# Kernel tuning notes

Hardware: AMD Instinct MI355X
Metric: run time of the kernel (lower is better)

The kernel has to match this reference:

```python
import jax, jax.numpy as jnp
import numpy as np

S, B, C, H, W = 16, 64, 128, 11, 11
P = H * W
N_ITER = 3
EPS = 1e-5


def setup_inputs() -> dict:
    key = jax.random.key(0)
    ks = jax.random.split(key, 12)
    w = lambda k, shape: jax.random.normal(k, shape, jnp.float32) * 0.02
    return {
        "x": jax.random.normal(ks[0], (S, B, C, H, W), jnp.float32),
        # intra-attention 1x1 convs (stored as [out,in] matrices)
        "wq": w(ks[1], (C, C)), "bq": jnp.zeros((C,), jnp.float32),
        "wk": w(ks[2], (C, C)), "bk": jnp.zeros((C,), jnp.float32),
        "wv": w(ks[3], (C, C)), "bv": jnp.zeros((C,), jnp.float32),
        "intra_alpha": jnp.float32(1.0),
        # inter-message path
        "w_msg": w(ks[4], (C, C + 1)), "b_msg": jnp.zeros((C,), jnp.float32),
        "w_lin": w(ks[5], (C, C)),
        "weight": jnp.float32(0.5),
        "w_gate": w(ks[6], (C, C)), "b_gate": jnp.zeros((C,), jnp.float32),
        # ConvGRU 3x3 convs
        "w_zr": w(ks[7], (2 * C, 2 * C, 3, 3)), "b_zr": jnp.zeros((2 * C,), jnp.float32),
        "w_h": w(ks[8], (C, 2 * C, 3, 3)), "b_h": jnp.zeros((C,), jnp.float32),
        # LayerNorm over [C,11,11]
        "ln_gamma": jnp.ones((C, H, W), jnp.float32),
        "ln_beta": jnp.zeros((C, H, W), jnp.float32),
    }


def reference(x, wq, bq, wk, bk, wv, bv, intra_alpha, w_msg, b_msg, w_lin,
              weight, w_gate, b_gate, w_zr, b_zr, w_h, b_h, ln_gamma, ln_beta):
    scale = C ** -0.5

    def c1(t, wgt, bias):  # 1x1 conv on [S,B,Cin,H,W] -> [S,B,Cout,H,W]
        return jnp.einsum('sbchw,oc->sbohw', t, wgt) + bias[:, None, None]

    def conv3(t, wgt, bias):  # 3x3 'SAME' conv on [N,Cin,H,W]
        y = jax.lax.conv_general_dilated(
            t, wgt, (1, 1), 'SAME', dimension_numbers=('NCHW', 'OIHW', 'NCHW'))
        return y + bias[None, :, None, None]

    # chain-graph neighbor validity masks (|i-j| == 1)
    mask_l = (jnp.arange(S) >= 1).astype(x.dtype)[:, None, None, None, None]
    mask_r = (jnp.arange(S) <= S - 2).astype(x.dtype)[:, None, None, None, None]

    h = x
    for _ in range(N_ITER):
        # ---- intra spatial self-attention (per node, over P=H*W tokens) ----
        q = c1(h, wq, bq).reshape(S, B, C, P)
        k = c1(h, wk, bk).reshape(S, B, C, P)
        v = c1(h, wv, bv).reshape(S, B, C, P)
        att = jax.nn.softmax(jnp.einsum('sbcp,sbcq->sbpq', q, k) * scale, axis=-1)
        intra = jnp.einsum('sbpq,sbcq->sbcp', att, v).reshape(S, B, C, H, W)
        intra = intra_alpha * intra + h

        # ---- inter gated message attention from chain neighbors ----
        xf = h.reshape(S, B, C, P)

        def gated_msg(y, edge_val):
            ef = jnp.full((S, B, 1, H, W), edge_val, h.dtype)  # edge feature i-j
            yy = c1(jnp.concatenate([y, ef], axis=2), w_msg, b_msg).reshape(S, B, C, P)
            yy = jnp.einsum('sbcp,dc->sbdp', yy, w_lin)  # Linear (no bias)
            a = jax.nn.softmax(jnp.einsum('sbcp,sbcq->sbpq', xf, yy), axis=-1)
            m = jnp.einsum('sbpq,sbcq->sbcp', a, yy).reshape(S, B, C, H, W)
            g = jax.nn.sigmoid(c1(m, w_gate, b_gate).mean(axis=(-2, -1), keepdims=True))
            return m * g

        y_left = jnp.concatenate([jnp.zeros_like(h[:1]), h[:-1]], axis=0)   # h[i-1], edge +1
        y_right = jnp.concatenate([h[1:], jnp.zeros_like(h[:1])], axis=0)   # h[i+1], edge -1
        inter = gated_msg(y_left, 1.0) * mask_l + gated_msg(y_right, -1.0) * mask_r

        comb = weight * intra + (1.0 - weight) * inter

        # ---- ConvGRU update (fold S into batch) ----
        xg = comb.reshape(S * B, C, H, W)
        hg = h.reshape(S * B, C, H, W)
        zr = jax.nn.sigmoid(conv3(jnp.concatenate([xg, hg], axis=1), w_zr, b_zr))
        z, r = zr[:, :C], zr[:, C:]
        h_hat = jnp.tanh(conv3(jnp.concatenate([xg, r * hg], axis=1), w_h, b_h))
        h_new = ((1 - z) * hg + z * h_hat).reshape(S, B, C, H, W)

        # ---- residual + LayerNorm over [C,H,W] ----
        nh = h_new + h
        mu = nh.mean(axis=(-3, -2, -1), keepdims=True)
        var = nh.var(axis=(-3, -2, -1), keepdims=True)
        h = (nh - mu) * jax.lax.rsqrt(var + EPS) * ln_gamma + ln_beta
    return h
```

## Files before the change

### kernel.cpp

```cpp
#include <hip/hip_runtime.h>
#include <hip/hip_bf16.h>

#define S_   16
#define B_   64
#define SBn  1024
#define C_   128
#define P_   121
#define CP_  15488
#define LTS  17408
static const long NEl = 15859712L;

typedef __hip_bfloat16 bf16t;
typedef __attribute__((ext_vector_type(8))) short bf16x8;
typedef __attribute__((ext_vector_type(4))) float f32x4;
typedef __attribute__((ext_vector_type(4))) unsigned short us4;

__device__ __forceinline__ float ldb(const bf16t* p){ return __bfloat162float(*p); }
__device__ __forceinline__ float b2f(unsigned short u){ unsigned x=((unsigned)u)<<16; float f; __builtin_memcpy(&f,&x,4); return f; }
__device__ __forceinline__ unsigned short f2bu(float v){ __hip_bfloat16 b=__float2bfloat16(v); unsigned short u; __builtin_memcpy(&u,&b,2); return u; }
__device__ __forceinline__ float ldin(const void* s, long i, int f){
    return f ? ((const float*)s)[i] : b2f(((const unsigned short*)s)[i]);
}

__global__ void detect_kernel(const unsigned short* __restrict__ x, int* __restrict__ flag){
// ... 264 lines not shown
    #pragma unroll
    for(int io=0;io<2;io++){
        f32x4 acc[4][2];
        gemm24r(acc,WqT,hreg[io],ocr,l15,kg);
        #pragma unroll
        for(int mt=0;mt<4;mt++){
            int oc0=ocr*64+mt*16+kg*4;
            #pragma unroll
            for(int nt=0;nt<2;nt++){
                int p=pcr*32+nt*16+l15;
                us4 pk;
                #pragma unroll
                for(int r=0;r<4;r++) pk[r]=f2bu(acc[mt][nt][r]+bq[oc0+r]);
                *(us4*)(LA[io]+p*136+oc0)=pk;
            }
        }
        gemm24r(acc,WkT,hreg[io],ocr,l15,kg);
        #pragma unroll
        for(int mt=0;mt<4;mt++){
            int oc0=ocr*64+mt*16+kg*4;
            #pragma unroll
            for(int nt=0;nt<2;nt++){
                int p=pcr*32+nt*16+l15;
                us4 pk;
                #pragma unroll
                for(int r=0;r<4;r++) pk[r]=f2bu(acc[mt][nt][r]+bk[oc0+r]);
                *(us4*)(LB[io]+p*136+oc0)=pk;
            }
        }
    }
    __syncthreads();
    const float scale=0.08838834764831845f;
    f32x4 s[2][8];
    #pragma unroll
    for(int io=0;io<2;io++){
        #pragma unroll
        for(int nt=0;nt<8;nt++) s[io][nt]=(f32x4){0.f,0.f,0.f,0.f};
        #pragma unroll
        for(int kc=0;kc<4;kc++){
            bf16x8 a=*(const bf16x8*)(LA[io]+(size_t)(m0+l15)*136+kc*32+kg*8);
            #pragma unroll
            for(int nt=0;nt<8;nt++){
                bf16x8 b=*(const bf16x8*)(LB[io]+(size_t)(nt*16+l15)*136+kc*32+kg*8);
                s[io][nt]=__builtin_amdgcn_mfma_f32_16x16x32_bf16(a,b,s[io][nt],0,0,0);
            }
        }
        #pragma unroll
        for(int nt=0;nt<8;nt++){
            #pragma unroll
            for(int r=0;r<4;r++) s[io][nt][r]*=scale;
        }
        if(l15>=9){
            #pragma unroll
            for(int r=0;r<4;r++) s[io][7][r]=-3.0e38f;
        }
        #pragma unroll
        for(int r=0;r<4;r++){
            float mx=s[io][0][r];
            #pragma unroll
            for(int nt=1;nt<8;nt++) mx=fmaxf(mx,s[io][nt][r]);
            #pragma unroll
            for(int o=1;o<16;o<<=1) mx=fmaxf(mx,__shfl_xor(mx,o));
            float sm=0.f;
            #pragma unroll
            for(int nt=0;nt<8;nt++){ float e=__expf(s[io][nt][r]-mx); s[io][nt][r]=e; sm+=e; }
            #pragma unroll
            for(int o=1;o<16;o<<=1) sm+=__shfl_xor(sm,o);
            float rs=1.f/sm;
            #pragma unroll
            for(int nt=0;nt<8;nt++) s[io][nt][r]*=rs;
        }
    }
    __syncthreads();
    #pragma unroll
    for(int io=0;io<2;io++){
        f32x4 acc[4][2];
        gemm24r(acc,WvT,hreg[io],ocr,l15,kg);
        #pragma unroll
        for(int mt=0;mt<4;mt++){
            int oc0=ocr*64+mt*16+kg*4;
            #pragma unroll
            for(int nt=0;nt<2;nt++){
                int p=pcr*32+nt*16+l15;
                #pragma unroll
                for(int r=0;r<4;r++)
                    LA[io][(oc0+r)*136+p]=__float2bfloat16(p<P_? acc[mt][nt][r]+bv[oc0+r] : 0.f);
            }
        }
        #pragma unroll
        for(int r=0;r<4;r++){
            int pr=m0+kg*4+r;
            #pragma unroll
            for(int nt=0;nt<8;nt++) LB[io][pr*136+nt*16+l15]=__float2bfloat16(s[io][nt][r]);
        }
    }
    __syncthreads();
    float al=*alphap, wv=*wp, w1m=1.f-wv;
    int c0=m0+kg*4;
    f32x4 res[2][8];
    #pragma unroll
    for(int io=0;io<2;io++){
        #pragma unroll
        for(int nt=0;nt<8;nt++) res[io][nt]=(f32x4){0.f,0.f,0.f,0.f};
        #pragma unroll
        for(int jc=0;jc<4;jc++){
            bf16x8 a=*(const bf16x8*)(LA[io]+(size_t)(m0+l15)*136+jc*32+kg*8);
            #pragma unroll
            for(int nt=0;nt<8;nt++){
                bf16x8 b=*(const bf16x8*)(LB[io]+(size_t)(nt*16+l15)*136+jc*32+kg*8);
                res[io][nt]=__builtin_amdgcn_mfma_f32_16x16x32_bf16(a,b,res[io][nt],0,0,0);
            }
        }
        const bf16t* hp=(io==0)?hp0:hp1;
        #pragma unroll
        for(int nt=0;nt<8;nt++){
            int p=nt*16+l15;
            int pc=(p<P_)?p:(P_-1);
            us4 hv=*(const us4*)(hp+(size_t)pc*C_+c0);
            #pragma unroll
            for(int r=0;r<4;r++) res[io][nt][r]=wv*(al*res[io][nt][r]+b2f(hv[r]));
        }
    }
    if(sb0>=B_)
        msg_phase2(res,hT,sb0,-B_,W2T,b2l,wgT,bgf,w1m,areg,LA,LB,fl,t,w,l15,kg,ocr,pcr);
    if(sb0<SBn-B_)
        msg_phase2(res,hT,sb0, B_,W2T,b2r,wgT,bgf,w1m,areg,LA,LB,fl,t,w,l15,kg,ocr,pcr);
    __syncthreads();
    #pragma unroll
    for(int io=0;io<2;io++){
        unsigned short* tl=(unsigned short*)LA[io];
        #pragma unroll
        for(int nt=0;nt<8;nt++){
            int p=nt*16+l15;
            if(p>=P_) continue;
            us4 pk;
            #pragma unroll
            for(int r=0;r<4;r++) pk[r]=f2bu(res[io][nt][r]);
            *(us4*)(tl+p*C_+c0)=pk;
        }
    }
    __syncthreads();
    {
        bf16t* ob0=comb+(size_t)sb0*CP_;
        const unsigned short* t0=(const unsigned short*)LA[0];
        for(int j=t;j<1936;j+=512)
            *(bf16x8*)(ob0+j*8)=*(const bf16x8*)(t0+j*8);
        bf16t* ob1=comb+(size_t)(sb0+1)*CP_;
        const unsigned short* t1=(const unsigned short*)LA[1];
        for(int j=t;j<1936;j+=512)
            *(bf16x8*)(ob1+j*8)=*(const bf16x8*)(t1+j*8);
    }
}

#define LOADA2(bidx, widx) { \
    _Pragma("unroll") \
    for(int mt=0;mt<2;mt++) abuf[bidx][mt]=*(const bf16x8*)(Wt+(size_t)(widx)*(OC*32)+mt*512+base_lane); }
#define STEP2(lbase, bidx, doff) { \
    bf16x8 bb[4]; \
    _Pragma("unroll") \
    for(int nt=0;nt<4;nt++) bb[nt]=*(const bf16x8*)((lbase)+boff[nt]+(doff)); \
    __builtin_amdgcn_s_setprio(1); \
    _Pragma("unroll") \
    for(int mt=0;mt<2;mt++){ \
        _Pragma("unroll") \
        for(int nt=0;nt<4;nt++) \
            acc[mt][nt]=__builtin_amdgcn_mfma_f32_16x16x32_bf16(abuf[bidx][mt],bb[nt],acc[mt][nt],0,0,0); } \
    __builtin_amdgcn_s_setprio(0); }

#define SLOADZ2(stg) { \
    const bf16t* s0=(((stg)<2)? in0T:in1T)+(size_t)sb0*CP_+((stg)&1)*64; \
    const bf16t* s1=s0+CP_; \
    sreg[0]=*(const bf16x8*)(s0+(size_t)spA*C_+(t&7)*8); \
    if(sv1) sreg[1]=*(const bf16x8*)(s0+(size_t)spB*C_+(t&7)*8); \
    sreg[2]=*(const bf16x8*)(s1+(size_t)spA*C_+(t&7)*8); \
    if(sv1) sreg[3]=*(const bf16x8*)(s1+(size_t)spB*C_+(t&7)*8); }
#define SWRITEZ2(lbase) { \
    *(bf16x8*)((lbase)+spixA*72+(t&7)*8)=sreg[0]; \
    if(sv1) *(bf16x8*)((lbase)+spixB*72+(t&7)*8)=sreg[1]; \
    *(bf16x8*)((lbase)+12176+spixA*72+(t&7)*8)=sreg[2]; \
    if(sv1) *(bf16x8*)((lbase)+12176+spixB*72+(t&7)*8)=sreg[3]; }
#define STEPZ2(lbase, bidx, doff) { \
    bf16x8 bb0[4], bb1[4]; \
    _Pragma("unroll") \
    for(int nt=0;nt<4;nt++){ \
        bb0[nt]=*(const bf16x8*)((lbase)+boff[nt]+(doff)); \
        bb1[nt]=*(const bf16x8*)((lbase)+12176+boff[nt]+(doff)); } \
    __builtin_amdgcn_s_setprio(1); \
    _Pragma("unroll") \
    for(int mt=0;mt<2;mt++){ \
        _Pragma("unroll") \
        for(int nt=0;nt<4;nt++){ \
            accA[mt][nt]=__builtin_amdgcn_mfma_f32_16x16x32_bf16(abuf[bidx][mt],bb0[nt],accA[mt][nt],0,0,0); \
            accB[mt][nt]=__builtin_amdgcn_mfma_f32_16x16x32_bf16(abuf[bidx][mt],bb1[nt],accB[mt][nt],0,0,0); } } \
    __builtin_amdgcn_s_setprio(0); }

__global__ __launch_bounds__(512) void conv3_zr2(
    bf16t* __restrict__ o0, bf16t* __restrict__ o1,
    const bf16t* __restrict__ in0T, const bf16t* __restrict__ in1T,
    const bf16t* __restrict__ Wt, const float* __restrict__ bias,
    const bf16t* __restrict__ hTb)
{
    constexpr int OC=256;
    __shared__ bf16t lin[4*12176];
    int sb0=(int)blockIdx.x*2, ocb=(int)blockIdx.y*128;
    int t=threadIdx.x, lane=t&63, w=t>>6;
    int ocr=w>>1, pcr=w&1, l15=lane&15, kg=lane>>4;
    int boff[4]; bool pv_[4];
    #pragma unroll
    for(int nt=0;nt<4;nt++){
        int p=pcr*64+nt*16+l15;
        pv_[nt]=(p<P_); int pc=pv_[nt]?p:(P_-1);
        boff[nt]=((pc/11)*13+(pc%11))*72+kg*8;
    }
    f32x4 accA[2][4], accB[2][4];
    #pragma unroll
    for(int i=0;i<2;i++){
        #pragma unroll
        for(int j=0;j<4;j++){ accA[i][j]=(f32x4){0.f,0.f,0.f,0.f}; accB[i][j]=(f32x4){0.f,0.f,0.f,0.f}; }
    }
    int base_lane=(ocb+ocr*32+l15)*32+kg*8;
    bf16x8 abuf[4][2];
    bf16x8 sreg[4];
    bool sv1=((t+512)<968);
    int spA=t>>3, spB=(t+512)>>3;
    if(spB>120) spB=120;
    int spixA=(spA/11+1)*13+(spA%11)+1;
    int spixB=(spB/11+1)*13+(spB%11)+1;
    LOADA2(0,0); LOADA2(1,1); LOADA2(2,8); LOADA2(3,9);
    SLOADZ2(0);
    {
        bf16x8 z;
        #pragma unroll
        for(int e=0;e<8;e++) z[e]=0;
        for(int i=t;i<1536;i+=512){
            int tile=i/384; int i2=i-tile*384;
            int bi=i2>>3, cc=(i2&7)*8;
            int pix;
            if(bi<13) pix=bi;
            else if(bi<26) pix=156+(bi-13);
            else { int j2=bi-26; pix=(1+(j2>>1))*13+((j2&1)?12:0); }
            *(bf16x8*)(lin+tile*12176+pix*72+cc)=z;
        }
    }
    SWRITEZ2(lin);
    __syncthreads();
    #pragma unroll
    for(int st=0; st<4; ++st){
        if(st<3) SLOADZ2(st+1);
        bf16t* lbase=lin+(st&1)*24352;
        #pragma unroll
        for(int k=0;k<18;k++){
            int s=st*18+k;
            int tap=k>>1, l=k&1;
            int doff=((tap/3)*13+(tap%3))*72+l*32;
            STEPZ2(lbase, s&3, doff);
            if(s<68){
                int s4=s+4, st4=s4/18, k4=s4-st4*18, tap4=k4>>1, l4=k4&1;
                LOADA2(s&3, tap4*8+st4*2+l4);
            }
        }
        if(st<3){ SWRITEZ2(lin+((st+1)&1)*24352); }
        __syncthreads();
    }
    unsigned short* tl=(unsigned short*)lin;
    bf16t* obase=(ocb==0? o0 : o1);
    const float* bs=bias+(ocb==0?0:128);
    #pragma unroll
    for(int mt=0;mt<2;mt++){
        int ocl=ocr*32+mt*16+kg*4;
        #pragma unroll
        for(int nt=0;nt<4;nt++){
            if(!pv_[nt]) continue;
            int p=pcr*64+nt*16+l15;
            us4 pk;
            if(ocb==0){
                #pragma unroll
                for(int r=0;r<4;r++){ float a=accA[mt][nt][r]+bs[ocl+r]; pk[r]=f2bu(1.f/(1.f+__expf(-a))); }
            }else{
                size_t tb=(size_t)sb0*CP_+(size_t)p*C_+ocl;
                us4 hv=*(const us4*)(hTb+tb);
                #pragma unroll
                for(int r=0;r<4;r++){ float a=accA[mt][nt][r]+bs[ocl+r]; float sg=1.f/(1.f+__expf(-a)); pk[r]=f2bu(sg*b2f(hv[r])); }
            }
            *(us4*)(tl+p*C_+ocl)=pk;
        }
    }
    __syncthreads();
    {
        bf16t* ob=obase+(size_t)sb0*CP_;
        for(int j=t;j<1936;j+=512)
            *(bf16x8*)(ob+j*8)=*(const bf16x8*)(tl+j*8);
    }
    __syncthreads();
    #pragma unroll
    for(int mt=0;mt<2;mt++){
        int ocl=ocr*32+mt*16+kg*4;
        #pragma unroll
        for(int nt=0;nt<4;nt++){
            if(!pv_[nt]) continue;
            int p=pcr*64+nt*16+l15;
            us4 pk;
            if(ocb==0){
                #pragma unroll
                for(int r=0;r<4;r++){ float a=accB[mt][nt][r]+bs[ocl+r]; pk[r]=f2bu(1.f/(1.f+__expf(-a))); }
            }else{
                size_t tb=(size_t)(sb0+1)*CP_+(size_t)p*C_+ocl;
                us4 hv=*(const us4*)(hTb+tb);
                #pragma unroll
                for(int r=0;r<4;r++){ float a=accB[mt][nt][r]+bs[ocl+r]; float sg=1.f/(1.f+__expf(-a)); pk[r]=f2bu(sg*b2f(hv[r])); }
            }
            *(us4*)(tl+p*C_+ocl)=pk;
        }
    }
    __syncthreads();
    {
        bf16t* ob=obase+(size_t)(sb0+1)*CP_;
        for(int j=t;j<1936;j+=512)
            *(bf16x8*)(ob+j*8)=*(const bf16x8*)(tl+j*8);
    }
}

#define SLOADH(stg) { \
    const bf16t* ssrc=(((stg)<2)? in0T:in1T)+(size_t)sb*CP_+((stg)&1)*64; \
    sreg[0]=*(const bf16x8*)(ssrc+(size_t)(t>>3)*C_+(t&7)*8); \
    if(sv1) sreg[1]=*(const bf16x8*)(ssrc+(size_t)sp1*C_+(t&7)*8); }
#define SWRITEH(lbase) { \
    *(bf16x8*)((lbase)+spix0*72+(t&7)*8)=sreg[0]; \
    if(sv1) *(bf16x8*)((lbase)+spix1*72+(t&7)*8)=sreg[1]; }

__global__ __launch_bounds__(512,4) void conv3_hh(
    bf16t* __restrict__ o0,
    const bf16t* __restrict__ in0T, const bf16t* __restrict__ in1T,
    const bf16t* __restrict__ Wt, const float* __restrict__ bias,
    const bf16t* __restrict__ zT, const bf16t* __restrict__ hTb,
    const float* __restrict__ gamT, const float* __restrict__ betT)
{
    constexpr int OC=128;
    __shared__ bf16t lin[2*12176];
    __shared__ float red[16];
    int sb=blockIdx.x;
    int t=threadIdx.x, lane=t&63, w=t>>6;
    int ocr=w>>1, pcr=w&1, l15=lane&15, kg=lane>>4;
    int boff[4]; bool pv_[4];
    #pragma unroll
    for(int nt=0;nt<4;nt++){
        int p=pcr*64+nt*16+l15;
        pv_[nt]=(p<P_); int pc=pv_[nt]?p:(P_-1);
        boff[nt]=((pc/11)*13+(pc%11))*72+kg*8;
    }
    f32x4 acc[2][4];
    #pragma unroll
    for(int i=0;i<2;i++){
        #pragma unroll
        for(int j=0;j<4;j++) acc[i][j]=(f32x4){0.f,0.f,0.f,0.f};
    }
    int base_lane=(ocr*32+l15)*32+kg*8;
    bf16x8 abuf[4][2];
    bf16x8 sreg[2];
    bool sv1=((t+512)<968);
    int sp0=t>>3, sp1=(t+512)>>3;
    if(sp1>120) sp1=120;
    int spix0=(sp0/11+1)*13+(sp0%11)+1;
    int spix1=(sp1/11+1)*13+(sp1%11)+1;
    LOADA2(0,0); LOADA2(1,1); LOADA2(2,8); LOADA2(3,9);
    SLOADH(0);
    {
        bf16x8 z;
        #pragma unroll
        for(int e=0;e<8;e++) z[e]=0;
        for(int i=t;i<768;i+=512){
            int half=i>=384; int i2=i-half*384;
            int bi=i2>>3, cc=(i2&7)*8;
            int pix;
            if(bi<13) pix=bi;
            else if(bi<26) pix=156+(bi-13);
            else { int j2=bi-26; pix=(1+(j2>>1))*13+((j2&1)?12:0); }
            *(bf16x8*)(lin+half*12176+pix*72+cc)=z;
        }
    }
    SWRITEH(lin);
    __syncthreads();
    #pragma unroll
    for(int st=0; st<4; ++st){
        if(st<3) SLOADH(st+1);
        bf16t* lbase=lin+(st&1)*12176;
        #pragma unroll
        for(int k=0;k<18;k++){
            int s=st*18+k;
            int tap=k>>1, l=k&1;
            int doff=((tap/3)*13+(tap%3))*72+l*32;
            STEP2(lbase, s&3, doff);
            if(s<68){
                int s4=s+4, st4=s4/18, k4=s4-st4*18, tap4=k4>>1, l4=k4&1;
                LOADA2(s&3, tap4*8+st4*2+l4);
            }
        }
        if(st<3){ SWRITEH(lin+((st+1)&1)*12176); }
        __syncthreads();
    }
    float ls=0.f, ls2=0.f;
    #pragma unroll
    for(int mt=0;mt<2;mt++){
        int ocl=ocr*32+mt*16+kg*4;
        #pragma unroll
        for(int nt=0;nt<4;nt++){
            if(!pv_[nt]) continue;
            int p=pcr*64+nt*16+l15;
            size_t tb=(size_t)sb*CP_+(size_t)p*C_+ocl;
            us4 hv=*(const us4*)(hTb+tb);
            us4 zv=*(const us4*)(zT+tb);
            us4 pk;
            #pragma unroll
            for(int r=0;r<4;r++){
                float a=acc[mt][nt][r]+bias[ocl+r];
                float ht=tanhf(a);
                float z=b2f(zv[r]), h=b2f(hv[r]);
                unsigned short u=f2bu((1.f-z)*h+z*ht+h);
                pk[r]=u;
                float nr=b2f(u); ls+=nr; ls2+=nr*nr;
            }
            *(us4*)((unsigned short*)lin + p*C_+ocl)=pk;
        }
    }
    #pragma unroll
    for(int o=32;o;o>>=1){ ls+=__shfl_xor(ls,o); ls2+=__shfl_xor(ls2,o); }
    if(lane==0){ red[w]=ls; red[8+w]=ls2; }
    __syncthreads();
    float Sx=0.f,Sx2=0.f;
    #pragma unroll
    for(int i=0;i<8;i++){ Sx+=red[i]; Sx2+=red[8+i]; }
    float mu=Sx*(1.f/(float)CP_);
    float var=Sx2*(1.f/(float)CP_)-mu*mu;
    float rstd=rsqrtf(var+1e-5f);
    bf16t* ho=o0+(size_t)sb*CP_;
    const unsigned short* tl=(const unsigned short*)lin;
    for(int j=t;j<1936;j+=512){
        int base=j*8;
        bf16x8 ovec;
        #pragma unroll
        for(int e=0;e<8;e++){
            float v=(b2f(tl[base+e])-mu)*rstd*gamT[base+e]+betT[base+e];
            ovec[e]=(short)f2bu(v);
        }
        *(bf16x8*)(ho+base)=ovec;
    }
}

__global__ __launch_bounds__(256) void finalT_kernel(void* __restrict__ fout, const bf16t* __restrict__ hT, const int* __restrict__ flag){
    __shared__ bf16t tl[CP_];
    int sb=blockIdx.x, t=threadIdx.x, f=*flag;
    for(int i=t;i<CP_;i+=256) tl[i]=hT[(size_t)sb*CP_+i];
    __syncthreads();
    for(int i=t;i<CP_;i+=256){
        int c=i/P_, p=i-c*P_;
        float v=ldb(tl+p*C_+c);
        size_t oi=(size_t)sb*CP_+i;
        if(f) ((float*)fout)[oi]=v;
        else  ((bf16t*)fout)[oi]=__float2bfloat16(v);
    }
}

extern "C" void kernel_launch(void* const* d_in, const int* in_sizes, int n_in,
                              void* d_out, int out_size, void* d_ws, size_t ws_size,
                              hipStream_t stream) {
    (void)in_sizes; (void)n_in; (void)out_size;
    char* base=(char*)d_ws;
    size_t off=0;
    auto alloc=[&](size_t bytes){ void* p=base+off; off+=(bytes+255)&~(size_t)255; return p; };
    bf16t* b1=(bf16t*)alloc((size_t)NEl*2+8192);
    bf16t* b2=(bf16t*)alloc((size_t)NEl*2+8192);
    bf16t* b3=(bf16t*)alloc((size_t)NEl*2+8192);
    bf16t* b4=(bf16t*)d_out;
    bf16t* wqT=(bf16t*)alloc(16384*2);
    bf16t* wkT=(bf16t*)alloc(16384*2);
    bf16t* wvT=(bf16t*)alloc(16384*2);
    bf16t* w2T=(bf16t*)alloc(16384*2);
    bf16t* wzrT=(bf16t*)alloc((size_t)589824*2);
    bf16t* whT =(bf16t*)alloc((size_t)294912*2);
    float* W2f=(float*)alloc(16384*4);
    float* b2l=(float*)alloc(128*4); float* b2r=(float*)alloc(128*4);
    float* bqf=(float*)alloc(128*4); float* bkf=(float*)alloc(128*4); float* bvf=(float*)alloc(128*4);
    float* bzrf=(float*)alloc(256*4); float* bhf=(float*)alloc(128*4);
    float* gamT=(float*)alloc(15488*4); float* betT=(float*)alloc(15488*4);
    float* wgTf=(float*)alloc(16384*4); float* bgf2=(float*)alloc(128*4);
    float* alphaf=(float*)alloc(4); float* weightf=(float*)alloc(4);
    int* flag=(int*)alloc(4);
    if(ws_size<off) return;

    detect_kernel<<<1,64,0,stream>>>((const unsigned short*)d_in[0],flag);
    cvtT_kernel<<<SBn,256,0,stream>>>(b1,d_in[0],flag);
    prep_w1t<1><<<64,256,0,stream>>>(wqT,d_in[1],flag);
    cvt_kernel<<<1,128,0,stream>>>(bqf,d_in[2],128,flag);
    prep_w1t<1><<<64,256,0,stream>>>(wkT,d_in[3],flag);
    cvt_kernel<<<1,128,0,stream>>>(bkf,d_in[4],128,flag);
    prep_w1t<1><<<64,256,0,stream>>>(wvT,d_in[5],flag);
    cvt_kernel<<<1,128,0,stream>>>(bvf,d_in[6],128,flag);
    cvt_kernel<<<1,64,0,stream>>>(alphaf,d_in[7],1,flag);
    prep_msg_kernel<<<C_,C_,0,stream>>>(W2f,b2l,b2r,d_in[10],d_in[8],d_in[9],flag);
    prep_w1t<0><<<64,256,0,stream>>>(w2T,W2f,flag);
    cvt_kernel<<<1,64,0,stream>>>(weightf,d_in[11],1,flag);
    prep_wgt<<<64,256,0,stream>>>(wgTf,bgf2,d_in[12],d_in[13],flag);
    prep_w3t<<<(256*2304+255)/256,256,0,stream>>>(wzrT,d_in[14],flag,256);
    cvt_kernel<<<1,256,0,stream>>>(bzrf,d_in[15],256,flag);
    prep_w3t<<<(128*2304+255)/256,256,0,stream>>>(whT,d_in[16],flag,128);
    cvt_kernel<<<1,128,0,stream>>>(bhf,d_in[17],128,flag);
    prep_gbt<<<(CP_+255)/256,256,0,stream>>>(gamT,betT,d_in[18],d_in[19],flag);

    for(int it=0; it<3; ++it){
        attn2<<<SBn/2,512,0,stream>>>(b2,b1,wqT,wkT,wvT,bqf,bkf,bvf,
                                      w2T,b2l,b2r,wgTf,bgf2,alphaf,weightf);
        conv3_zr2<<<dim3(SBn/2,2),512,0,stream>>>(b4,b3,b2,b1,wzrT,bzrf,b1);
        conv3_hh<<<SBn,512,0,stream>>>(b1,b2,b3,whT,bhf,b4,b1,gamT,betT);
    }
    finalT_kernel<<<SBn,256,0,stream>>>(d_out,b1,flag);
}
```

Baseline: 1.300 ms.

## Process two nodes per block in the h-hat conv to reuse weight fragments

After: 1.286 ms. About the same (-1.0%).

```diff
diff --git a/kernel.cpp b/kernel.cpp
--- a/kernel.cpp
+++ b/kernel.cpp
@@ -443,18 +443,6 @@
 #define LOADA2(bidx, widx) { \
     _Pragma("unroll") \
     for(int mt=0;mt<2;mt++) abuf[bidx][mt]=*(const bf16x8*)(Wt+(size_t)(widx)*(OC*32)+mt*512+base_lane); }
-#define STEP2(lbase, bidx, doff) { \
-    bf16x8 bb[4]; \
-    _Pragma("unroll") \
-    for(int nt=0;nt<4;nt++) bb[nt]=*(const bf16x8*)((lbase)+boff[nt]+(doff)); \
-    __builtin_amdgcn_s_setprio(1); \
-    _Pragma("unroll") \
-    for(int mt=0;mt<2;mt++){ \
-        _Pragma("unroll") \
-        for(int nt=0;nt<4;nt++) \
-            acc[mt][nt]=__builtin_amdgcn_mfma_f32_16x16x32_bf16(abuf[bidx][mt],bb[nt],acc[mt][nt],0,0,0); } \
-    __builtin_amdgcn_s_setprio(0); }
-
 #define SLOADZ2(stg) { \
     const bf16t* s0=(((stg)<2)? in0T:in1T)+(size_t)sb0*CP_+((stg)&1)*64; \
     const bf16t* s1=s0+CP_; \
@@ -608,15 +596,7 @@
     }
 }
 
-#define SLOADH(stg) { \
-    const bf16t* ssrc=(((stg)<2)? in0T:in1T)+(size_t)sb*CP_+((stg)&1)*64; \
-    sreg[0]=*(const bf16x8*)(ssrc+(size_t)(t>>3)*C_+(t&7)*8); \
-    if(sv1) sreg[1]=*(const bf16x8*)(ssrc+(size_t)sp1*C_+(t&7)*8); }
-#define SWRITEH(lbase) { \
-    *(bf16x8*)((lbase)+spix0*72+(t&7)*8)=sreg[0]; \
-    if(sv1) *(bf16x8*)((lbase)+spix1*72+(t&7)*8)=sreg[1]; }
-
-__global__ __launch_bounds__(512,4) void conv3_hh(
+__global__ __launch_bounds__(512) void conv3_hh2(
     bf16t* __restrict__ o0,
     const bf16t* __restrict__ in0T, const bf16t* __restrict__ in1T,
     const bf16t* __restrict__ Wt, const float* __restrict__ bias,
@@ -624,9 +604,9 @@
     const float* __restrict__ gamT, const float* __restrict__ betT)
 {
     constexpr int OC=128;
-    __shared__ bf16t lin[2*12176];
+    __shared__ bf16t lin[4*12176];
     __shared__ float red[16];
-    int sb=blockIdx.x;
+    int sb0=(int)blockIdx.x*2;
     int t=threadIdx.x, lane=t&63, w=t>>6;
     int ocr=w>>1, pcr=w&1, l15=lane&15, kg=lane>>4;
     int boff[4]; bool pv_[4];
@@ -636,101 +616,151 @@
         pv_[nt]=(p<P_); int pc=pv_[nt]?p:(P_-1);
         boff[nt]=((pc/11)*13+(pc%11))*72+kg*8;
     }
-    f32x4 acc[2][4];
+    f32x4 accA[2][4], accB[2][4];
     #pragma unroll
     for(int i=0;i<2;i++){
         #pragma unroll
-        for(int j=0;j<4;j++) acc[i][j]=(f32x4){0.f,0.f,0.f,0.f};
+        for(int j=0;j<4;j++){ accA[i][j]=(f32x4){0.f,0.f,0.f,0.f}; accB[i][j]=(f32x4){0.f,0.f,0.f,0.f}; }
     }
     int base_lane=(ocr*32+l15)*32+kg*8;
     bf16x8 abuf[4][2];
-    bf16x8 sreg[2];
+    bf16x8 sreg[4];
     bool sv1=((t+512)<968);
-    int sp0=t>>3, sp1=(t+512)>>3;
-    if(sp1>120) sp1=120;
-    int spix0=(sp0/11+1)*13+(sp0%11)+1;
-    int spix1=(sp1/11+1)*13+(sp1%11)+1;
+    int spA=t>>3, spB=(t+512)>>3;
+    if(spB>120) spB=120;
+    int spixA=(spA/11+1)*13+(spA%11)+1;
+    int spixB=(spB/11+1)*13+(spB%11)+1;
     LOADA2(0,0); LOADA2(1,1); LOADA2(2,8); LOADA2(3,9);
-    SLOADH(0);
+    SLOADZ2(0);
     {
         bf16x8 z;
         #pragma unroll
         for(int e=0;e<8;e++) z[e]=0;
-        for(int i=t;i<768;i+=512){
-            int half=i>=384; int i2=i-half*384;
+        for(int i=t;i<1536;i+=512){
+            int tile=i/384; int i2=i-tile*384;
             int bi=i2>>3, cc=(i2&7)*8;
             int pix;
             if(bi<13) pix=bi;
             else if(bi<26) pix=156+(bi-13);
             else { int j2=bi-26; pix=(1+(j2>>1))*13+((j2&1)?12:0); }
-            *(bf16x8*)(lin+half*12176+pix*72+cc)=z;
-        }
-    }
-    SWRITEH(lin);
+            *(bf16x8*)(lin+tile*12176+pix*72+cc)=z;
+        }
+    }
+    SWRITEZ2(lin);
     __syncthreads();
     #pragma unroll
     for(int st=0; st<4; ++st){
-        if(st<3) SLOADH(st+1);
-        bf16t* lbase=lin+(st&1)*12176;
+        if(st<3) SLOADZ2(st+1);
+        bf16t* lbase=lin+(st&1)*24352;
         #pragma unroll
         for(int k=0;k<18;k++){
             int s=st*18+k;
             int tap=k>>1, l=k&1;
             int doff=((tap/3)*13+(tap%3))*72+l*32;
-            STEP2(lbase, s&3, doff);
+            STEPZ2(lbase, s&3, doff);
             if(s<68){
                 int s4=s+4, st4=s4/18, k4=s4-st4*18, tap4=k4>>1, l4=k4&1;
                 LOADA2(s&3, tap4*8+st4*2+l4);
             }
         }
-        if(st<3){ SWRITEH(lin+((st+1)&1)*12176); }
+        if(st<3){ SWRITEZ2(lin+((st+1)&1)*24352); }
         __syncthreads();
     }
-    float ls=0.f, ls2=0.f;
-    #pragma unroll
-    for(int mt=0;mt<2;mt++){
-        int ocl=ocr*32+mt*16+kg*4;
-        #pragma unroll
-        for(int nt=0;nt<4;nt++){
-            if(!pv_[nt]) continue;
-            int p=pcr*64+nt*16+l15;
-            size_t tb=(size_t)sb*CP_+(size_t)p*C_+ocl;
-            us4 hv=*(const us4*)(hTb+tb);
-            us4 zv=*(const us4*)(zT+tb);
-            us4 pk;
-            #pragma unroll
-            for(int r=0;r<4;r++){
-                float a=acc[mt][nt][r]+bias[ocl+r];
-                float ht=tanhf(a);
-                float z=b2f(zv[r]), h=b2f(hv[r]);
-                unsigned short u=f2bu((1.f-z)*h+z*ht+h);
-                pk[r]=u;
-                float nr=b2f(u); ls+=nr; ls2+=nr*nr;
-            }
-            *(us4*)((unsigned short*)lin + p*C_+ocl)=pk;
-        }
-    }
-    #pragma unroll
-    for(int o=32;o;o>>=1){ ls+=__shfl_xor(ls,o); ls2+=__shfl_xor(ls2,o); }
-    if(lane==0){ red[w]=ls; red[8+w]=ls2; }
-    __syncthreads();
-    float Sx=0.f,Sx2=0.f;
-    #pragma unroll
-    for(int i=0;i<8;i++){ Sx+=red[i]; Sx2+=red[8+i]; }
-    float mu=Sx*(1.f/(float)CP_);
-    float var=Sx2*(1.f/(float)CP_)-mu*mu;
-    float rstd=rsqrtf(var+1e-5f);
-    bf16t* ho=o0+(size_t)sb*CP_;
-    const unsigned short* tl=(const unsigned short*)lin;
-    for(int j=t;j<1936;j+=512){
-        int base=j*8;
-        bf16x8 ovec;
-        #pragma unroll
-        for(int e=0;e<8;e++){
-            float v=(b2f(tl[base+e])-mu)*rstd*gamT[base+e]+betT[base+e];
-            ovec[e]=(short)f2bu(v);
-        }
-        *(bf16x8*)(ho+base)=ovec;
+    unsigned short* tl=(unsigned short*)lin;
+    {
+        float ls=0.f, ls2=0.f;
+        #pragma unroll
+        for(int mt=0;mt<2;mt++){
+            int ocl=ocr*32+mt*16+kg*4;
+            #pragma unroll
+            for(int nt=0;nt<4;nt++){
+                if(!pv_[nt]) continue;
+                int p=pcr*64+nt*16+l15;
+                size_t tb=(size_t)sb0*CP_+(size_t)p*C_+ocl;
+                us4 hv=*(const us4*)(hTb+tb);
+                us4 zv=*(const us4*)(zT+tb);
+                us4 pk;
+                #pragma unroll
+                for(int r=0;r<4;r++){
+                    float a=accA[mt][nt][r]+bias[ocl+r];
+                    float ht=tanhf(a);
+                    float z=b2f(zv[r]), h=b2f(hv[r]);
+                    unsigned short u=f2bu((1.f-z)*h+z*ht+h);
+                    pk[r]=u;
+                    float nr=b2f(u); ls+=nr; ls2+=nr*nr;
+                }
+                *(us4*)(tl+p*C_+ocl)=pk;
+            }
+        }
+        #pragma unroll
+        for(int o=32;o;o>>=1){ ls+=__shfl_xor(ls,o); ls2+=__shfl_xor(ls2,o); }
+        if(lane==0){ red[w]=ls; red[8+w]=ls2; }
+        __syncthreads();
+        float Sx=0.f,Sx2=0.f;
+        #pragma unroll
+        for(int i=0;i<8;i++){ Sx+=red[i]; Sx2+=red[8+i]; }
+        float mu=Sx*(1.f/(float)CP_);
+        float var=Sx2*(1.f/(float)CP_)-mu*mu;
+        float rstd=rsqrtf(var+1e-5f);
+        bf16t* ho=o0+(size_t)sb0*CP_;
+        for(int j=t;j<1936;j+=512){
+            int base=j*8;
+            bf16x8 ovec;
+            #pragma unroll
+            for(int e=0;e<8;e++){
+                float v=(b2f(tl[base+e])-mu)*rstd*gamT[base+e]+betT[base+e];
+                ovec[e]=(short)f2bu(v);
+            }
+            *(bf16x8*)(ho+base)=ovec;
+        }
+    }
+    __syncthreads();
+    {
+        float ls=0.f, ls2=0.f;
+        #pragma unroll
+        for(int mt=0;mt<2;mt++){
+            int ocl=ocr*32+mt*16+kg*4;
+            #pragma unroll
+            for(int nt=0;nt<4;nt++){
+                if(!pv_[nt]) continue;
+                int p=pcr*64+nt*16+l15;
+                size_t tb=(size_t)(sb0+1)*CP_+(size_t)p*C_+ocl;
+                us4 hv=*(const us4*)(hTb+tb);
+                us4 zv=*(const us4*)(zT+tb);
+                us4 pk;
+                #pragma unroll
+                for(int r=0;r<4;r++){
+                    float a=accB[mt][nt][r]+bias[ocl+r];
+                    float ht=tanhf(a);
+                    float z=b2f(zv[r]), h=b2f(hv[r]);
+                    unsigned short u=f2bu((1.f-z)*h+z*ht+h);
+                    pk[r]=u;
+                    float nr=b2f(u); ls+=nr; ls2+=nr*nr;
+                }
+                *(us4*)(tl+p*C_+ocl)=pk;
+            }
+        }
+        #pragma unroll
+        for(int o=32;o;o>>=1){ ls+=__shfl_xor(ls,o); ls2+=__shfl_xor(ls2,o); }
+        if(lane==0){ red[w]=ls; red[8+w]=ls2; }
+        __syncthreads();
+        float Sx=0.f,Sx2=0.f;
+        #pragma unroll
+        for(int i=0;i<8;i++){ Sx+=red[i]; Sx2+=red[8+i]; }
+        float mu=Sx*(1.f/(float)CP_);
+        float var=Sx2*(1.f/(float)CP_)-mu*mu;
+        float rstd=rsqrtf(var+1e-5f);
+        bf16t* ho=o0+(size_t)(sb0+1)*CP_;
+        for(int j=t;j<1936;j+=512){
+            int base=j*8;
+            bf16x8 ovec;
+            #pragma unroll
+            for(int e=0;e<8;e++){
+                float v=(b2f(tl[base+e])-mu)*rstd*gamT[base+e]+betT[base+e];
+                ovec[e]=(short)f2bu(v);
+            }
+            *(bf16x8*)(ho+base)=ovec;
+        }
     }
 }
 
@@ -798,7 +828,7 @@
         attn2<<<SBn/2,512,0,stream>>>(b2,b1,wqT,wkT,wvT,bqf,bkf,bvf,
                                       w2T,b2l,b2r,wgTf,bgf2,alphaf,weightf);
         conv3_zr2<<<dim3(SBn/2,2),512,0,stream>>>(b4,b3,b2,b1,wzrT,bzrf,b1);
-        conv3_hh<<<SBn,512,0,stream>>>(b1,b2,b3,whT,bhf,b4,b1,gamT,betT);
+        conv3_hh2<<<SBn/2,512,0,stream>>>(b1,b2,b3,whT,bhf,b4,b1,gamT,betT);
     }
     finalT_kernel<<<SBn,256,0,stream>>>(d_out,b1,flag);
 }
```

## Fuse ConvGRU gate and candidate convolutions into one kernel via LDS

Applied to the files above, without the earlier changes.

New measurement: 1.253 ms. -3.6%, faster.

```diff
diff --git a/kernel.cpp b/kernel.cpp
--- a/kernel.cpp
+++ b/kernel.cpp
@@ -440,82 +440,81 @@
     }
 }
 
-#define LOADA2(bidx, widx) { \
+#define GSB0 0
+#define GSB1 12176
+#define GSP0 24352
+#define GSP1 36528
+#define GSZ  48704
+#define SZSTR 132
+
+#define LOADAZ(bidx, widx) { \
     _Pragma("unroll") \
-    for(int mt=0;mt<2;mt++) abuf[bidx][mt]=*(const bf16x8*)(Wt+(size_t)(widx)*(OC*32)+mt*512+base_lane); }
-#define STEP2(lbase, bidx, doff) { \
+    for(int mt=0;mt<2;mt++) abuf[bidx][mt]=*(const bf16x8*)(Wzr+(size_t)(widx)*(256*32)+mt*512+base_laneZ); }
+#define LOADAH(bidx, widx) { \
+    _Pragma("unroll") \
+    for(int mt=0;mt<2;mt++) abuf[bidx][mt]=*(const bf16x8*)(Wh+(size_t)(widx)*(128*32)+mt*512+base_laneH); }
+#define STEPZ8(lbase, bidx, doff) { \
+    bf16x8 bb[8]; \
+    _Pragma("unroll") \
+    for(int nt=0;nt<8;nt++) bb[nt]=*(const bf16x8*)(lin+(lbase)+boffZ[nt]+(doff)); \
+    __builtin_amdgcn_s_setprio(1); \
+    _Pragma("unroll") \
+    for(int mt=0;mt<2;mt++){ \
+        _Pragma("unroll") \
+        for(int nt=0;nt<8;nt++) \
+            accZ[mt][nt]=__builtin_amdgcn_mfma_f32_16x16x32_bf16(abuf[bidx][mt],bb[nt],accZ[mt][nt],0,0,0); } \
+    __builtin_amdgcn_s_setprio(0); }
+#define STEPH4(lbase, bidx, doff) { \
     bf16x8 bb[4]; \
     _Pragma("unroll") \
-    for(int nt=0;nt<4;nt++) bb[nt]=*(const bf16x8*)((lbase)+boff[nt]+(doff)); \
+    for(int nt=0;nt<4;nt++) bb[nt]=*(const bf16x8*)(lin+(lbase)+boffH[nt]+(doff)); \
     __builtin_amdgcn_s_setprio(1); \
     _Pragma("unroll") \
     for(int mt=0;mt<2;mt++){ \
         _Pragma("unroll") \
         for(int nt=0;nt<4;nt++) \
-            acc[mt][nt]=__builtin_amdgcn_mfma_f32_16x16x32_bf16(abuf[bidx][mt],bb[nt],acc[mt][nt],0,0,0); } \
+            accH[mt][nt]=__builtin_amdgcn_mfma_f32_16x16x32_bf16(abuf[bidx][mt],bb[nt],accH[mt][nt],0,0,0); } \
     __builtin_amdgcn_s_setprio(0); }
-
-#define SLOADZ2(stg) { \
-    const bf16t* s0=(((stg)<2)? in0T:in1T)+(size_t)sb0*CP_+((stg)&1)*64; \
-    const bf16t* s1=s0+CP_; \
-    sreg[0]=*(const bf16x8*)(s0+(size_t)spA*C_+(t&7)*8); \
-    if(sv1) sreg[1]=*(const bf16x8*)(s0+(size_t)spB*C_+(t&7)*8); \
-    sreg[2]=*(const bf16x8*)(s1+(size_t)spA*C_+(t&7)*8); \
-    if(sv1) sreg[3]=*(const bf16x8*)(s1+(size_t)spB*C_+(t&7)*8); }
-#define SWRITEZ2(lbase) { \
-    *(bf16x8*)((lbase)+spixA*72+(t&7)*8)=sreg[0]; \
-    if(sv1) *(bf16x8*)((lbase)+spixB*72+(t&7)*8)=sreg[1]; \
-    *(bf16x8*)((lbase)+12176+spixA*72+(t&7)*8)=sreg[2]; \
-    if(sv1) *(bf16x8*)((lbase)+12176+spixB*72+(t&7)*8)=sreg[3]; }
-#define STEPZ2(lbase, bidx, doff) { \
-    bf16x8 bb0[4], bb1[4]; \
-    _Pragma("unroll") \
-    for(int nt=0;nt<4;nt++){ \
-        bb0[nt]=*(const bf16x8*)((lbase)+boff[nt]+(doff)); \
-        bb1[nt]=*(const bf16x8*)((lbase)+12176+boff[nt]+(doff)); } \
-    __builtin_amdgcn_s_setprio(1); \
-    _Pragma("unroll") \
-    for(int mt=0;mt<2;mt++){ \
-        _Pragma("unroll") \
-        for(int nt=0;nt<4;nt++){ \
-            accA[mt][nt]=__builtin_amdgcn_mfma_f32_16x16x32_bf16(abuf[bidx][mt],bb0[nt],accA[mt][nt],0,0,0); \
-            accB[mt][nt]=__builtin_amdgcn_mfma_f32_16x16x32_bf16(abuf[bidx][mt],bb1[nt],accB[mt][nt],0,0,0); } } \
-    __builtin_amdgcn_s_setprio(0); }
-
-__global__ __launch_bounds__(512) void conv3_zr2(
-    bf16t* __restrict__ o0, bf16t* __restrict__ o1,
-    const bf16t* __restrict__ in0T, const bf16t* __restrict__ in1T,
-    const bf16t* __restrict__ Wt, const float* __restrict__ bias,
-    const bf16t* __restrict__ hTb)
+#define SLOADG(srcp) { \
+    sreg[0]=*(const bf16x8*)((srcp)+(size_t)spA*C_+(t&7)*8); \
+    if(sv1) sreg[1]=*(const bf16x8*)((srcp)+(size_t)spB*C_+(t&7)*8); }
+#define SWRITEG(lbase) { \
+    *(bf16x8*)(lin+(lbase)+spixA*72+(t&7)*8)=sreg[0]; \
+    if(sv1) *(bf16x8*)(lin+(lbase)+spixB*72+(t&7)*8)=sreg[1]; }
+
+__global__ __launch_bounds__(512) void gru_fused(
+    bf16t* __restrict__ hTout, const bf16t* __restrict__ comb, const bf16t* __restrict__ hTb,
+    const bf16t* __restrict__ Wzr, const float* __restrict__ bzr,
+    const bf16t* __restrict__ Wh, const float* __restrict__ bh,
+    const float* __restrict__ gamT, const float* __restrict__ betT)
 {
-    constexpr int OC=256;
-    __shared__ bf16t lin[4*12176];
-    int sb0=(int)blockIdx.x*2, ocb=(int)blockIdx.y*128;
-    int t=threadIdx.x, lane=t&63, w=t>>6;
-    int ocr=w>>1, pcr=w&1, l15=lane&15, kg=lane>>4;
-    int boff[4]; bool pv_[4];
-    #pragma unroll
-    for(int nt=0;nt<4;nt++){
-        int p=pcr*64+nt*16+l15;
-        pv_[nt]=(p<P_); int pc=pv_[nt]?p:(P_-1);
-        boff[nt]=((pc/11)*13+(pc%11))*72+kg*8;
-    }
-    f32x4 accA[2][4], accB[2][4];
-    #pragma unroll
-    for(int i=0;i<2;i++){
-        #pragma unroll
-        for(int j=0;j<4;j++){ accA[i][j]=(f32x4){0.f,0.f,0.f,0.f}; accB[i][j]=(f32x4){0.f,0.f,0.f,0.f}; }
-    }
-    int base_lane=(ocb+ocr*32+l15)*32+kg*8;
-    bf16x8 abuf[4][2];
-    bf16x8 sreg[4];
+    __shared__ bf16t lin[64704];
+    __shared__ float red[16];
+    int sb=blockIdx.x, t=threadIdx.x, lane=t&63, w=t>>6;
+    int l15=lane&15, kg=lane>>4;
+    bf16x8 sreg[2];
     bool sv1=((t+512)<968);
     int spA=t>>3, spB=(t+512)>>3;
     if(spB>120) spB=120;
     int spixA=(spA/11+1)*13+(spA%11)+1;
     int spixB=(spB/11+1)*13+(spB%11)+1;
-    LOADA2(0,0); LOADA2(1,1); LOADA2(2,8); LOADA2(3,9);
-    SLOADZ2(0);
+    int boffZ[8]; bool pvZ[8];
+    #pragma unroll
+    for(int nt=0;nt<8;nt++){
+        int p=nt*16+l15;
+        pvZ[nt]=(p<P_); int pc=pvZ[nt]?p:(P_-1);
+        boffZ[nt]=((pc/11)*13+(pc%11))*72+kg*8;
+    }
+    f32x4 accZ[2][8];
+    #pragma unroll
+    for(int i=0;i<2;i++){
+        #pragma unroll
+        for(int j=0;j<8;j++) accZ[i][j]=(f32x4){0.f,0.f,0.f,0.f};
+    }
+    int base_laneZ=(w*32+l15)*32+kg*8;
+    bf16x8 abuf[4][2];
+    LOADAZ(0,0); LOADAZ(1,1); LOADAZ(2,8); LOADAZ(3,9);
+    SLOADG(comb+(size_t)sb*CP_);
     {
         bf16x8 z;
         #pragma unroll
@@ -530,184 +529,132 @@
             *(bf16x8*)(lin+tile*12176+pix*72+cc)=z;
         }
     }
-    SWRITEZ2(lin);
+    SWRITEG(GSB0);
     __syncthreads();
     #pragma unroll
     for(int st=0; st<4; ++st){
-        if(st<3) SLOADZ2(st+1);
-        bf16t* lbase=lin+(st&1)*24352;
+        if(st<3){
+            const bf16t* nsrc=((st+1)<2? comb:hTb)+(size_t)sb*CP_+((st+1)&1)*64;
+            SLOADG(nsrc);
+        }
+        int lbase=(st&1)? GSB1:GSB0;
         #pragma unroll
         for(int k=0;k<18;k++){
             int s=st*18+k;
             int tap=k>>1, l=k&1;
             int doff=((tap/3)*13+(tap%3))*72+l*32;
-            STEPZ2(lbase, s&3, doff);
+            STEPZ8(lbase, s&3, doff);
             if(s<68){
                 int s4=s+4, st4=s4/18, k4=s4-st4*18, tap4=k4>>1, l4=k4&1;
-                LOADA2(s&3, tap4*8+st4*2+l4);
-            }
-        }
-        if(st<3){ SWRITEZ2(lin+((st+1)&1)*24352); }
+                LOADAZ(s&3, tap4*8+st4*2+l4);
+            }
+        }
+        if(st<3){ SWRITEG(((st+1)&1)? GSB1:GSB0); }
         __syncthreads();
     }
-    unsigned short* tl=(unsigned short*)lin;
-    bf16t* obase=(ocb==0? o0 : o1);
-    const float* bs=bias+(ocb==0?0:128);
-    #pragma unroll
-    for(int mt=0;mt<2;mt++){
-        int ocl=ocr*32+mt*16+kg*4;
-        #pragma unroll
-        for(int nt=0;nt<4;nt++){
-            if(!pv_[nt]) continue;
-            int p=pcr*64+nt*16+l15;
-            us4 pk;
-            if(ocb==0){
+    if(w<4){
+        #pragma unroll
+        for(int mt=0;mt<2;mt++){
+            int oc=w*32+mt*16+kg*4;
+            #pragma unroll
+            for(int nt=0;nt<8;nt++){
+                if(!pvZ[nt]) continue;
+                int p=nt*16+l15;
+                us4 pk;
                 #pragma unroll
-                for(int r=0;r<4;r++){ float a=accA[mt][nt][r]+bs[ocl+r]; pk[r]=f2bu(1.f/(1.f+__expf(-a))); }
-            }else{
-                size_t tb=(size_t)sb0*CP_+(size_t)p*C_+ocl;
-                us4 hv=*(const us4*)(hTb+tb);
+                for(int r=0;r<4;r++){ float a=accZ[mt][nt][r]+bzr[oc+r]; pk[r]=f2bu(1.f/(1.f+__expf(-a))); }
+                *(us4*)(lin+GSZ+p*SZSTR+oc)=pk;
+            }
+        }
+    }else{
+        int icb=w-4;
+        #pragma unroll
+        for(int mt=0;mt<2;mt++){
+            int ic=icb*32+mt*16+kg*4;
+            int tb=(ic<64)? GSP0:GSP1;
+            int icl=ic&63;
+            #pragma unroll
+            for(int nt=0;nt<8;nt++){
+                if(!pvZ[nt]) continue;
+                int p=nt*16+l15;
+                int pixE=(p/11+1)*13+(p%11)+1;
+                us4 hv=*(const us4*)(hTb+(size_t)sb*CP_+(size_t)p*C_+ic);
+                us4 pk;
                 #pragma unroll
-                for(int r=0;r<4;r++){ float a=accA[mt][nt][r]+bs[ocl+r]; float sg=1.f/(1.f+__expf(-a)); pk[r]=f2bu(sg*b2f(hv[r])); }
-            }
-            *(us4*)(tl+p*C_+ocl)=pk;
-        }
-    }
-    __syncthreads();
-    {
-        bf16t* ob=obase+(size_t)sb0*CP_;
-        for(int j=t;j<1936;j+=512)
-            *(bf16x8*)(ob+j*8)=*(const bf16x8*)(tl+j*8);
-    }
-    __syncthreads();
-    #pragma unroll
-    for(int mt=0;mt<2;mt++){
-        int ocl=ocr*32+mt*16+kg*4;
-        #pragma unroll
-        for(int nt=0;nt<4;nt++){
-            if(!pv_[nt]) continue;
-            int p=pcr*64+nt*16+l15;
-            us4 pk;
-            if(ocb==0){
-                #pragma unroll
-                for(int r=0;r<4;r++){ float a=accB[mt][nt][r]+bs[ocl+r]; pk[r]=f2bu(1.f/(1.f+__expf(-a))); }
-            }else{
-                size_t tb=(size_t)(sb0+1)*CP_+(size_t)p*C_+ocl;
-                us4 hv=*(const us4*)(hTb+tb);
-                #pragma unroll
-                for(int r=0;r<4;r++){ float a=accB[mt][nt][r]+bs[ocl+r]; float sg=1.f/(1.f+__expf(-a)); pk[r]=f2bu(sg*b2f(hv[r])); }
-            }
-            *(us4*)(tl+p*C_+ocl)=pk;
-        }
-    }
-    __syncthreads();
-    {
-        bf16t* ob=obase+(size_t)(sb0+1)*CP_;
-        for(int j=t;j<1936;j+=512)
-            *(bf16x8*)(ob+j*8)=*(const bf16x8*)(tl+j*8);
-    }
-}
-
-#define SLOADH(stg) { \
-    const bf16t* ssrc=(((stg)<2)? in0T:in1T)+(size_t)sb*CP_+((stg)&1)*64; \
-    sreg[0]=*(const bf16x8*)(ssrc+(size_t)(t>>3)*C_+(t&7)*8); \
-    if(sv1) sreg[1]=*(const bf16x8*)(ssrc+(size_t)sp1*C_+(t&7)*8); }
-#define SWRITEH(lbase) { \
-    *(bf16x8*)((lbase)+spix0*72+(t&7)*8)=sreg[0]; \
-    if(sv1) *(bf16x8*)((lbase)+spix1*72+(t&7)*8)=sreg[1]; }
-
-__global__ __launch_bounds__(512,4) void conv3_hh(
-    bf16t* __restrict__ o0,
-    const bf16t* __restrict__ in0T, const bf16t* __restrict__ in1T,
-    const bf16t* __restrict__ Wt, const float* __restrict__ bias,
-    const bf16t* __restrict__ zT, const bf16t* __restrict__ hTb,
-    const float* __restrict__ gamT, const float* __restrict__ betT)
-{
-    constexpr int OC=128;
-    __shared__ bf16t lin[2*12176];
-    __shared__ float red[16];
-    int sb=blockIdx.x;
-    int t=threadIdx.x, lane=t&63, w=t>>6;
-    int ocr=w>>1, pcr=w&1, l15=lane&15, kg=lane>>4;
-    int boff[4]; bool pv_[4];
+                for(int r=0;r<4;r++){
+                    float a=accZ[mt][nt][r]+bzr[128+ic+r];
+                    float sg=1.f/(1.f+__expf(-a));
+                    pk[r]=f2bu(sg*b2f(hv[r]));
+                }
+                *(us4*)(lin+tb+pixE*72+icl)=pk;
+            }
+        }
+    }
+    __syncthreads();
+    int ocrH=w>>1, pcrH=w&1;
+    int boffH[4]; bool pvH[4];
     #pragma unroll
     for(int nt=0;nt<4;nt++){
-        int p=pcr*64+nt*16+l15;
-        pv_[nt]=(p<P_); int pc=pv_[nt]?p:(P_-1);
-        boff[nt]=((pc/11)*13+(pc%11))*72+kg*8;
-    }
-    f32x4 acc[2][4];
+        int p=pcrH*64+nt*16+l15;
+        pvH[nt]=(p<P_); int pc=pvH[nt]?p:(P_-1);
+        boffH[nt]=((pc/11)*13+(pc%11))*72+kg*8;
+    }
+    f32x4 accH[2][4];
     #pragma unroll
     for(int i=0;i<2;i++){
         #pragma unroll
-        for(int j=0;j<4;j++) acc[i][j]=(f32x4){0.f,0.f,0.f,0.f};
-    }
-    int base_lane=(ocr*32+l15)*32+kg*8;
-    bf16x8 abuf[4][2];
-    bf16x8 sreg[2];
-    bool sv1=((t+512)<968);
-    int sp0=t>>3, sp1=(t+512)>>3;
-    if(sp1>120) sp1=120;
-    int spix0=(sp0/11+1)*13+(sp0%11)+1;
-    int spix1=(sp1/11+1)*13+(sp1%11)+1;
-    LOADA2(0,0); LOADA2(1,1); LOADA2(2,8); LOADA2(3,9);
-    SLOADH(0);
-    {
-        bf16x8 z;
-        #pragma unroll
-        for(int e=0;e<8;e++) z[e]=0;
-        for(int i=t;i<768;i+=512){
-            int half=i>=384; int i2=i-half*384;
-            int bi=i2>>3, cc=(i2&7)*8;
-            int pix;
-            if(bi<13) pix=bi;
-            else if(bi<26) pix=156+(bi-13);
-            else { int j2=bi-26; pix=(1+(j2>>1))*13+((j2&1)?12:0); }
-            *(bf16x8*)(lin+half*12176+pix*72+cc)=z;
-        }
-    }
-    SWRITEH(lin);
-    __syncthreads();
-    #pragma unroll
-    for(int st=0; st<4; ++st){
-        if(st<3) SLOADH(st+1);
-        bf16t* lbase=lin+(st&1)*12176;
+        for(int j=0;j<4;j++) accH[i][j]=(f32x4){0.f,0.f,0.f,0.f};
+    }
+    int base_laneH=(ocrH*32+l15)*32+kg*8;
+    LOADAH(0,4); LOADAH(1,5); LOADAH(2,12); LOADAH(3,13);
+    SLOADG(comb+(size_t)sb*CP_);
+    #pragma unroll
+    for(int sidx=0; sidx<4; ++sidx){
+        if(sidx==2){
+            SWRITEG(GSB0);
+            SLOADG(comb+(size_t)sb*CP_+64);
+            __syncthreads();
+        }
+        if(sidx==3){
+            SWRITEG(GSB1);
+            __syncthreads();
+        }
+        int lbase=(sidx==0)?GSP0:(sidx==1)?GSP1:(sidx==2)?GSB0:GSB1;
         #pragma unroll
         for(int k=0;k<18;k++){
-            int s=st*18+k;
+            int s=sidx*18+k;
             int tap=k>>1, l=k&1;
             int doff=((tap/3)*13+(tap%3))*72+l*32;
-            STEP2(lbase, s&3, doff);
+            STEPH4(lbase, s&3, doff);
             if(s<68){
-                int s4=s+4, st4=s4/18, k4=s4-st4*18, tap4=k4>>1, l4=k4&1;
-                LOADA2(s&3, tap4*8+st4*2+l4);
-            }
-        }
-        if(st<3){ SWRITEH(lin+((st+1)&1)*12176); }
-        __syncthreads();
-    }
+                int s4=s+4, sidx4=s4/18, k4=s4-sidx4*18, tap4=k4>>1, l4=k4&1;
+                int st4=(sidx4<2)?(2+sidx4):(sidx4-2);
+                LOADAH(s&3, tap4*8+st4*2+l4);
+            }
+        }
+    }
+    __syncthreads();
     float ls=0.f, ls2=0.f;
     #pragma unroll
     for(int mt=0;mt<2;mt++){
-        int ocl=ocr*32+mt*16+kg*4;
+        int oc=ocrH*32+mt*16+kg*4;
         #pragma unroll
         for(int nt=0;nt<4;nt++){
-            if(!pv_[nt]) continue;
-            int p=pcr*64+nt*16+l15;
-            size_t tb=(size_t)sb*CP_+(size_t)p*C_+ocl;
-            us4 hv=*(const us4*)(hTb+tb);
-            us4 zv=*(const us4*)(zT+tb);
+            if(!pvH[nt]) continue;
+            int p=pcrH*64+nt*16+l15;
+            us4 hv=*(const us4*)(hTb+(size_t)sb*CP_+(size_t)p*C_+oc);
+            us4 zv=*(const us4*)(lin+GSZ+p*SZSTR+oc);
             us4 pk;
             #pragma unroll
             for(int r=0;r<4;r++){
-                float a=acc[mt][nt][r]+bias[ocl+r];
+                float a=accH[mt][nt][r]+bh[oc+r];
                 float ht=tanhf(a);
                 float z=b2f(zv[r]), h=b2f(hv[r]);
                 unsigned short u=f2bu((1.f-z)*h+z*ht+h);
                 pk[r]=u;
                 float nr=b2f(u); ls+=nr; ls2+=nr*nr;
             }
-            *(us4*)((unsigned short*)lin + p*C_+ocl)=pk;
+            *(us4*)((unsigned short*)lin + p*C_+oc)=pk;
         }
     }
     #pragma unroll
@@ -720,7 +667,7 @@
     float mu=Sx*(1.f/(float)CP_);
     float var=Sx2*(1.f/(float)CP_)-mu*mu;
     float rstd=rsqrtf(var+1e-5f);
-    bf16t* ho=o0+(size_t)sb*CP_;
+    bf16t* ho=hTout+(size_t)sb*CP_;
     const unsigned short* tl=(const unsigned short*)lin;
     for(int j=t;j<1936;j+=512){
         int base=j*8;
@@ -757,8 +704,6 @@
     auto alloc=[&](size_t bytes){ void* p=base+off; off+=(bytes+255)&~(size_t)255; return p; };
     bf16t* b1=(bf16t*)alloc((size_t)NEl*2+8192);
     bf16t* b2=(bf16t*)alloc((size_t)NEl*2+8192);
-    bf16t* b3=(bf16t*)alloc((size_t)NEl*2+8192);
-    bf16t* b4=(bf16t*)d_out;
     bf16t* wqT=(bf16t*)alloc(16384*2);
     bf16t* wkT=(bf16t*)alloc(16384*2);
     bf16t* wvT=(bf16t*)alloc(16384*2);
@@ -797,8 +742,7 @@
     for(int it=0; it<3; ++it){
         attn2<<<SBn/2,512,0,stream>>>(b2,b1,wqT,wkT,wvT,bqf,bkf,bvf,
                                       w2T,b2l,b2r,wgTf,bgf2,alphaf,weightf);
-        conv3_zr2<<<dim3(SBn/2,2),512,0,stream>>>(b4,b3,b2,b1,wzrT,bzrf,b1);
-        conv3_hh<<<SBn,512,0,stream>>>(b1,b2,b3,whT,bhf,b4,b1,gamT,betT);
+        gru_fused<<<SBn,512,0,stream>>>(b1,b2,b1,wzrT,bzrf,whT,bhf,gamT,betT);
     }
     finalT_kernel<<<SBn,256,0,stream>>>(d_out,b1,flag);
 }
```
